# Kernel optimization log

Measured on AMD Instinct MI355X. Metric: run time of the kernel, lower is better.

The kernel has to match this reference:

```python
import jax, jax.numpy as jnp
import numpy as np

N_NODES = 100000
N_EDGES = 1600000
IN_DIM, HID_DIM, OUT_DIM = 128, 256, 128


def gcn_conv(x, src, dst, W, b, n):
    # PyG GCNConv: linear transform, add self-loops, symmetric normalization,
    # scatter-sum aggregation over destination nodes, then bias.
    h = x @ W  # [n, d_out]
    loops = jnp.arange(n, dtype=src.dtype)
    s = jnp.concatenate([src, loops])
    d = jnp.concatenate([dst, loops])
    deg = jax.ops.segment_sum(jnp.ones_like(d, dtype=h.dtype), d, num_segments=n)
    dinv = jnp.where(deg > 0, jax.lax.rsqrt(deg), 0.0)
    norm = dinv[s] * dinv[d]  # [E+n]
    msg = h[s] * norm[:, None]  # gather + scale
    out = jax.ops.segment_sum(msg, d, num_segments=n)  # scatter-reduce
    return out + b


def layer_norm(x, gamma, beta, eps=1e-5):
    mu = jnp.mean(x, axis=-1, keepdims=True)
    var = jnp.mean(jnp.square(x - mu), axis=-1, keepdims=True)
    return (x - mu) * jax.lax.rsqrt(var + eps) * gamma + beta


def setup_inputs() -> dict:
    key = jax.random.key(0)
    ks = jax.random.split(key, 8)
    x = jax.random.normal(ks[0], (N_NODES, IN_DIM), dtype=jnp.float32)
    edge_index = jax.random.randint(ks[1], (2, N_EDGES), 0, N_NODES, dtype=jnp.int64)
    W1 = jax.random.normal(ks[2], (IN_DIM, HID_DIM), dtype=jnp.float32) * (1.0 / np.sqrt(IN_DIM))
    b1 = jnp.zeros((HID_DIM,), dtype=jnp.float32)
    W2 = jax.random.normal(ks[3], (HID_DIM, OUT_DIM), dtype=jnp.float32) * (1.0 / np.sqrt(HID_DIM))
    b2 = jnp.zeros((OUT_DIM,), dtype=jnp.float32)
    gamma = jnp.ones((OUT_DIM,), dtype=jnp.float32)
    beta = jnp.zeros((OUT_DIM,), dtype=jnp.float32)
    return {"x": x, "edge_index": edge_index, "W1": W1, "b1": b1,
            "W2": W2, "b2": b2, "gamma": gamma, "beta": beta}


def reference(x, edge_index, W1, b1, W2, b2, gamma, beta):
    n = x.shape[0]
    src, dst = edge_index[0], edge_index[1]
    h = gcn_conv(x, src, dst, W1, b1, n)
    h = jax.nn.relu(h)
    # dropout(p=0.1) is identity in eval mode
    h = gcn_conv(h, src, dst, W2, b2, n)
    return layer_norm(h, gamma, beta)
```

## Files before the change

### kernel.cpp

```cpp
#include <hip/hip_runtime.h>
#include <hip/hip_fp16.h>
#include <stdint.h>

#define N_NODES 100000
#define N_EDGES 1600000
#define IN_DIM  128
#define HID_DIM 256
#define OUT_DIM 128
#define RS 264
#define NBUCK 782
#define EPB   4096
#define PADB  2816
#define RPT   11
#define PB    391
#define WB    256

typedef __attribute__((ext_vector_type(8))) _Float16 f16x8;
typedef __attribute__((ext_vector_type(4))) float f32x4;

__device__ __forceinline__ int clampi(int v) {
    v = v < 0 ? 0 : v;
    return v >= N_NODES ? N_NODES - 1 : v;
}
__device__ __forceinline__ float2 h2f2(uint32_t u) {
    union { uint32_t u; __half2 h; } c; c.u = u;
    return __half22float2(c.h);
}
__device__ __forceinline__ uint32_t packh(float a, float b) {
    union { __half2 h; uint32_t u; } c; c.h = __floats2half2_rn(a, b);
    return c.u;
}
__device__ __forceinline__ uint16_t f2h(float a) {
    union { __half h; uint16_t s; } c; c.h = __float2half_rn(a);
    return c.s;
}

__device__ __forceinline__ int src_at(const int* ei, int isI64, int e) {
    return clampi(isI64 ? ei[2 * (size_t)e] : ei[e]);
}
__device__ __forceinline__ int dst_at(const int* ei, int isI64, int e) {
    return clampi(isI64 ? ei[2 * (size_t)N_EDGES + 2 * (size_t)e]
                        : ei[(size_t)N_EDGES + e]);
}


__global__ __launch_bounds__(256) void partition_kernel(const int* __restrict__ ei,
                                                        int* __restrict__ cursor,
                                                        uint32_t* __restrict__ recs,
                                                        const float* __restrict__ W1,
                                                        uint16_t* __restrict__ W1t,
                                                        const float* __restrict__ W2,
                                                        uint16_t* __restrict__ W2t) {
    if (blockIdx.x >= PB) {
        int idx = (blockIdx.x - PB) * 256 + threadIdx.x;
        if (idx < IN_DIM * HID_DIM) {
            int k = idx / HID_DIM, n = idx - k * HID_DIM;
            W1t[n * IN_DIM + k] = f2h(W1[idx]);
        } else {
            int j = idx - IN_DIM * HID_DIM;
            int k = j / OUT_DIM, n = j - k * OUT_DIM;
            W2t[n * HID_DIM + k] = f2h(W2[j]);
        }
        return;
    }
    __shared__ int hist[NBUCK];
    __shared__ int gBase[NBUCK];
    __shared__ int s_flag;
    int tid = threadIdx.x;
    if (tid == 0) {
        int z = 1;
        #pragma unroll
        for (int i = 0; i < 16; ++i)
            if (ei[2 * i + 1] != 0) z = 0;
        s_flag = z;
    }
    for (int b = tid; b < NBUCK; b += 256) hist[b] = 0;
    __syncthreads();
    int isI64 = s_flag;
    int base = blockIdx.x * EPB;
    int srcs[16], dsts[16], slots[16];
    #pragma unroll
    for (int r = 0; r < 16; ++r) {
        int e = base + r * 256 + tid;
        slots[r] = -1;
        srcs[r] = 0; dsts[r] = 0;
        if (e < N_EDGES) {
            srcs[r] = src_at(ei, isI64, e);
            dsts[r] = dst_at(ei, isI64, e);
            slots[r] = atomicAdd(&hist[dsts[r] >> 7], 1);
        }
    }
    __syncthreads();
    for (int b = tid; b < NBUCK; b += 256)
        if (hist[b] > 0) gBase[b] = atomicAdd(&cursor[b], hist[b]);
    __syncthreads();
    #pragma unroll
    for (int r = 0; r < 16; ++r) {
        if (slots[r] >= 0) {
            int b = dsts[r] >> 7;
            int pos = gBase[b] + slots[r];
            if (pos < PADB)
                recs[(size_t)b * PADB + pos] =
                    ((uint32_t)srcs[r] << 7) | (uint32_t)(dsts[r] & 127);
        }
    }
}


__global__ __launch_bounds__(256) void build_kernel(const uint32_t* __restrict__ recs,
                                                    const int* __restrict__ cursor,
                                                    int* __restrict__ row_ptr,
                                                    float* __restrict__ dinv,
                                                    int* __restrict__ colv) {
    __shared__ int cnt[128];
    __shared__ int lofs[128];
    __shared__ int cur[128];
    __shared__ int wsum[8];
    int b = blockIdx.x, tid = threadIdx.x;
    int lane = tid & 63, wv = tid >> 6;
    int nb = cursor[b]; if (nb > PADB) nb = PADB;
    int pv = 0;
    for (int j = tid; j < b; j += 256) {
        int c = cursor[j];
        pv += (c > PADB) ? PADB : c;
    }
    #pragma unroll
    for (int o = 32; o > 0; o >>= 1) pv += __shfl_xor(pv, o, 64);
    if (tid < 128) { cnt[tid] = 0; cur[tid] = 0; }
    if (lane == 0) wsum[wv] = pv;
    __syncthreads();
    int cbase = wsum[0] + wsum[1] + wsum[2] + wsum[3];
    uint32_t rr[RPT];
    #pragma unroll
    for (int r = 0; r < RPT; ++r) {
        int i = r * 256 + tid;
        rr[r] = 0xFFFFFFFFu;
        if (i < nb) {
            rr[r] = recs[(size_t)b * PADB + i];
            atomicAdd(&cnt[rr[r] & 127], 1);
        }
    }
    __syncthreads();
    int v = (tid < 128) ? cnt[tid] : 0;
    int inc = v;
    #pragma unroll
    for (int o = 1; o < 64; o <<= 1) {
        int t = __shfl_up(inc, o, 64);
        if (lane >= o) inc += t;
    }
    if (lane == 63) wsum[4 + wv] = inc;
    __syncthreads();
    int woff = 0;
    #pragma unroll
    for (int w = 0; w < 4; ++w) if (w < wv) woff += wsum[4 + w];
    int excl = woff + inc - v;
    int node = b * 128 + tid;
    if (tid < 128) {
        lofs[tid] = excl;
        if (node < N_NODES) {
            row_ptr[node] = cbase + excl;
            dinv[node] = rsqrtf((float)(v + 1));
        }
    }
    if (b == NBUCK - 1 && tid == 0) row_ptr[N_NODES] = cbase + nb;
    __syncthreads();
    #pragma unroll
    for (int r = 0; r < RPT; ++r) {
        if (rr[r] != 0xFFFFFFFFu) {
            int id = (int)(rr[r] & 127);
            int slot = atomicAdd(&cur[id], 1);
            colv[cbase + lofs[id] + slot] = (int)(rr[r] >> 7);
        }
    }
}


__global__ __launch_bounds__(256) void xscale_kernel(const float* __restrict__ x,
                                                     const float* __restrict__ dinv,
                                                     uint2* __restrict__ xs16) {
    int idx = blockIdx.x * 256 + threadIdx.x;
    if (idx < N_NODES * 32) {
        float d = dinv[idx >> 5];
        float4 v = ((const float4*)x)[idx];
        uint2 o;
        o.x = packh(d * v.x, d * v.y);
        o.y = packh(d * v.z, d * v.w);
        xs16[idx] = o;
    }
}


template<bool LN>
__global__ __launch_bounds__(256) void agg_kernel(const uint4* __restrict__ rows,
                                                  const int* __restrict__ row_ptr,
                                                  const int* __restrict__ colv,
                                                  const float* __restrict__ dinv,
                                                  const float* __restrict__ bias,
                                                  const float* __restrict__ gamma,
                                                  const float* __restrict__ beta,
                                                  float* __restrict__ out,
                                                  uint4* __restrict__ out16) {
    int node = blockIdx.x * 16 + (threadIdx.x >> 4);
    if (node >= N_NODES) return;
    int l = threadIdx.x & 15;
    const char* base = (const char*)rows + ((unsigned)l << 4);
    float di = dinv[node];
    float acc[8];
    {
        uint4 u = *(const uint4*)(base + ((unsigned)node << 8));
        float2 f0 = h2f2(u.x), f1 = h2f2(u.y), f2 = h2f2(u.z), f3 = h2f2(u.w);
        acc[0] = f0.x; acc[1] = f0.y; acc[2] = f1.x; acc[3] = f1.y;
        acc[4] = f2.x; acc[5] = f2.y; acc[6] = f3.x; acc[7] = f3.y;
    }
    int e = row_ptr[node], e1 = row_ptr[node + 1];
    int s0 = 0, s1 = 0, s2 = 0, s3 = 0;
    if (e     < e1) s0 = colv[e];
    if (e + 1 < e1) s1 = colv[e + 1];
    if (e + 2 < e1) s2 = colv[e + 2];
    if (e + 3 < e1) s3 = colv[e + 3];
    while (e + 4 <= e1) {
        uint4 v0 = *(const uint4*)(base + ((unsigned)s0 << 8));
        uint4 v1 = *(const uint4*)(base + ((unsigned)s1 << 8));
        uint4 v2 = *(const uint4*)(base + ((unsigned)s2 << 8));
        uint4 v3 = *(const uint4*)(base + ((unsigned)s3 << 8));
        int p0 = (e + 4 < e1) ? e + 4 : e;
        int p1 = (e + 5 < e1) ? e + 5 : e;
        int p2 = (e + 6 < e1) ? e + 6 : e;
        int p3 = (e + 7 < e1) ? e + 7 : e;
        int t0 = colv[p0], t1 = colv[p1], t2 = colv[p2], t3 = colv[p3];
        {
            float2 f0 = h2f2(v0.x), f1 = h2f2(v0.y), f2 = h2f2(v0.z), f3 = h2f2(v0.w);
            acc[0] += f0.x; acc[1] += f0.y; acc[2] += f1.x; acc[3] += f1.y;
            acc[4] += f2.x; acc[5] += f2.y; acc[6] += f3.x; acc[7] += f3.y;
        }
        {
            float2 f0 = h2f2(v1.x), f1 = h2f2(v1.y), f2 = h2f2(v1.z), f3 = h2f2(v1.w);
            acc[0] += f0.x; acc[1] += f0.y; acc[2] += f1.x; acc[3] += f1.y;
            acc[4] += f2.x; acc[5] += f2.y; acc[6] += f3.x; acc[7] += f3.y;
        }
        {
            float2 f0 = h2f2(v2.x), f1 = h2f2(v2.y), f2 = h2f2(v2.z), f3 = h2f2(v2.w);
            acc[0] += f0.x; acc[1] += f0.y; acc[2] += f1.x; acc[3] += f1.y;
            acc[4] += f2.x; acc[5] += f2.y; acc[6] += f3.x; acc[7] += f3.y;
        }
        {
            float2 f0 = h2f2(v3.x), f1 = h2f2(v3.y), f2 = h2f2(v3.z), f3 = h2f2(v3.w);
            acc[0] += f0.x; acc[1] += f0.y; acc[2] += f1.x; acc[3] += f1.y;
            acc[4] += f2.x; acc[5] += f2.y; acc[6] += f3.x; acc[7] += f3.y;
        }
        s0 = t0; s1 = t1; s2 = t2; s3 = t3; e += 4;
    }
    int r = e1 - e;
    if (r > 0) {
        uint4 v = *(const uint4*)(base + ((unsigned)s0 << 8));
        float2 f0 = h2f2(v.x), f1 = h2f2(v.y), f2 = h2f2(v.z), f3 = h2f2(v.w);
        acc[0] += f0.x; acc[1] += f0.y; acc[2] += f1.x; acc[3] += f1.y;
        acc[4] += f2.x; acc[5] += f2.y; acc[6] += f3.x; acc[7] += f3.y;
    }
    if (r > 1) {
        uint4 v = *(const uint4*)(base + ((unsigned)s1 << 8));
        float2 f0 = h2f2(v.x), f1 = h2f2(v.y), f2 = h2f2(v.z), f3 = h2f2(v.w);
        acc[0] += f0.x; acc[1] += f0.y; acc[2] += f1.x; acc[3] += f1.y;
        acc[4] += f2.x; acc[5] += f2.y; acc[6] += f3.x; acc[7] += f3.y;
    }
    if (r > 2) {
        uint4 v = *(const uint4*)(base + ((unsigned)s2 << 8));
        float2 f0 = h2f2(v.x), f1 = h2f2(v.y), f2 = h2f2(v.z), f3 = h2f2(v.w);
        acc[0] += f0.x; acc[1] += f0.y; acc[2] += f1.x; acc[3] += f1.y;
        acc[4] += f2.x; acc[5] += f2.y; acc[6] += f3.x; acc[7] += f3.y;
    }
    if (!LN) {
        uint4 o;
        o.x = packh(acc[0] * di, acc[1] * di);
        o.y = packh(acc[2] * di, acc[3] * di);
        o.z = packh(acc[4] * di, acc[5] * di);
        o.w = packh(acc[6] * di, acc[7] * di);
        out16[(size_t)node * 16 + l] = o;
    } else {
        const float4* b4 = (const float4*)(bias + l * 8);
        float4 bb0 = b4[0], bb1 = b4[1];
        float v[8];
        v[0] = acc[0] * di + bb0.x; v[1] = acc[1] * di + bb0.y;
        v[2] = acc[2] * di + bb0.z; v[3] = acc[3] * di + bb0.w;
        v[4] = acc[4] * di + bb1.x; v[5] = acc[5] * di + bb1.y;
        v[6] = acc[6] * di + bb1.z; v[7] = acc[7] * di + bb1.w;
        float s = 0.f;
        #pragma unroll
        for (int j = 0; j < 8; ++j) s += v[j];
        #pragma unroll
        for (int o = 8; o > 0; o >>= 1) s += __shfl_xor(s, o, 64);
        float mu = s * (1.0f / 128.0f);
        float q = 0.f;
        #pragma unroll
        for (int j = 0; j < 8; ++j) { v[j] -= mu; q += v[j] * v[j]; }
        #pragma unroll
        for (int o = 8; o > 0; o >>= 1) q += __shfl_xor(q, o, 64);
        float rstd = rsqrtf(q * (1.0f / 128.0f) + 1e-5f);
        const float4* g4 = (const float4*)(gamma + l * 8);
        const float4* t4 = (const float4*)(beta + l * 8);
        float4 g0 = g4[0], g1 = g4[1], t0 = t4[0], t1 = t4[1];
        float* orow = out + (size_t)node * 128 + l * 8;
        f32x4 o0, o1;
        o0.x = v[0] * rstd * g0.x + t0.x; o0.y = v[1] * rstd * g0.y + t0.y;
        o0.z = v[2] * rstd * g0.z + t0.z; o0.w = v[3] * rstd * g0.w + t0.w;
        o1.x = v[4] * rstd * g1.x + t1.x; o1.y = v[5] * rstd * g1.y + t1.y;
        o1.z = v[6] * rstd * g1.z + t1.z; o1.w = v[7] * rstd * g1.w + t1.w;
        __builtin_nontemporal_store(o0, (f32x4*)orow);
        __builtin_nontemporal_store(o1, (f32x4*)(orow + 4));
    }
}


__global__ __launch_bounds__(256) void fused_gemm_kernel(const uint16_t* __restrict__ A16,
                                                         const uint16_t* __restrict__ W1t,
                                                         const float* __restrict__ b1,
                                                         const uint16_t* __restrict__ W2t,
                                                         const float* __restrict__ dinv,
                                                         uint16_t* __restrict__ G16, int M) {
    __shared__ __align__(16) uint16_t Hs[64 * RS];
    int lane = threadIdx.x & 63;
    int wave = threadIdx.x >> 6;
    int r15 = lane & 15;
    int quad = lane >> 4;
    int kofs = quad * 8;
    int blk_row = blockIdx.x * 64;

    f16x8 a[4][4];
    #pragma unroll
    for (int mt = 0; mt < 4; ++mt) {
        bool valid = (blk_row + mt * 16) < M;
        int row = valid ? (blk_row + mt * 16 + r15) : 0;
        const uint16_t* arow = A16 + (size_t)row * IN_DIM + kofs;
        #pragma unroll
        for (int ks = 0; ks < 4; ++ks)
            a[mt][ks] = *(const f16x8*)(arow + ks * 32);
    }

    #pragma unroll
    for (int nt = 0; nt < 4; ++nt) {
        int ncol = (wave * 4 + nt) * 16 + r15;
        const uint16_t* bp = W1t + (size_t)ncol * IN_DIM + kofs;
        f32x4 acc[4];
        #pragma unroll
        for (int mt = 0; mt < 4; ++mt) acc[mt] = (f32x4){0.f, 0.f, 0.f, 0.f};
        #pragma unroll
        for (int ks = 0; ks < 4; ++ks) {
            f16x8 bv = *(const f16x8*)(bp + ks * 32);
            #pragma unroll
            for (int mt = 0; mt < 4; ++mt)
                acc[mt] = __builtin_amdgcn_mfma_f32_16x16x32_f16(a[mt][ks], bv, acc[mt], 0, 0, 0);
        }
        float bb = b1[ncol];
        #pragma unroll
        for (int mt = 0; mt < 4; ++mt) {
            #pragma unroll
            for (int r = 0; r < 4; ++r) {
                int lrow = mt * 16 + quad * 4 + r;
                Hs[lrow * RS + ncol] = f2h(fmaxf(acc[mt][r] + bb, 0.f));
            }
        }
    }
    __syncthreads();

    #pragma unroll
    for (int nt = 0; nt < 2; ++nt) {
        int ncol = (wave * 2 + nt) * 16 + r15;
        const uint16_t* bp = W2t + (size_t)ncol * HID_DIM + kofs;
        f16x8 b2[8];
        #pragma unroll
        for (int ks = 0; ks < 8; ++ks)
            b2[ks] = *(const f16x8*)(bp + ks * 32);
        f32x4 acc[4];
        #pragma unroll
        for (int mt = 0; mt < 4; ++mt) acc[mt] = (f32x4){0.f, 0.f, 0.f, 0.f};
        #pragma unroll
        for (int ks = 0; ks < 8; ++ks) {
            #pragma unroll
            for (int mt = 0; mt < 4; ++mt) {
                f16x8 av = *(const f16x8*)(Hs + (mt * 16 + r15) * RS + ks * 32 + kofs);
                acc[mt] = __builtin_amdgcn_mfma_f32_16x16x32_f16(av, b2[ks], acc[mt], 0, 0, 0);
            }
        }
        #pragma unroll
        for (int mt = 0; mt < 4; ++mt) {
            if ((blk_row + mt * 16) < M) {
                #pragma unroll
                for (int r = 0; r < 4; ++r) {
                    int row = blk_row + mt * 16 + quad * 4 + r;
                    G16[(size_t)row * OUT_DIM + ncol] = f2h(dinv[row] * acc[mt][r]);
                }
            }
        }
    }
}


extern "C" void kernel_launch(void* const* d_in, const int* in_sizes, int n_in,
                              void* d_out, int out_size, void* d_ws, size_t ws_size,
                              hipStream_t stream) {
    const float* x     = (const float*)d_in[0];
    const int*   ei    = (const int*)d_in[1];
    const float* W1    = (const float*)d_in[2];
    const float* b1    = (const float*)d_in[3];
    const float* W2    = (const float*)d_in[4];
    const float* b2    = (const float*)d_in[5];
    const float* gamma = (const float*)d_in[6];
    const float* beta  = (const float*)d_in[7];

    char* ws = (char*)d_ws;
    size_t off = 0;
    auto alloc = [&](size_t bytes) -> void* {
        void* p = ws + off;
        off += (bytes + 511) & ~(size_t)511;
        return p;
    };
    int*      cursor  = (int*)alloc((size_t)NBUCK * 4);
    int*      row_ptr = (int*)alloc((size_t)(N_NODES + 1) * 4);
    float*    dinv    = (float*)alloc((size_t)N_NODES * 4);
    uint16_t* W1t     = (uint16_t*)alloc((size_t)IN_DIM * HID_DIM * 2);
    uint16_t* W2t     = (uint16_t*)alloc((size_t)HID_DIM * OUT_DIM * 2);
    int*      colv    = (int*)alloc((size_t)N_EDGES * 4);
    void*     big     = alloc((size_t)N_NODES * IN_DIM * 2);
    uint32_t* recs    = (uint32_t*)big;
    uint16_t* g16     = (uint16_t*)big;
    if (ws_size < off) return;

    uint2*    xs16 = (uint2*)d_out;
    uint16_t* xa16 = (uint16_t*)d_out + (size_t)N_NODES * IN_DIM;

    const int AB = (N_NODES + 15) / 16;
    const int GB = (N_NODES + 63) / 64;
    const int XB = (N_NODES * 32 + 255) / 256;

    hipMemsetAsync(cursor, 0, (size_t)NBUCK * 4, stream);
    partition_kernel<<<PB + WB, 256, 0, stream>>>(ei, cursor, recs, W1, W1t, W2, W2t);
    build_kernel<<<NBUCK, 256, 0, stream>>>(recs, cursor, row_ptr, dinv, colv);
    xscale_kernel<<<XB, 256, 0, stream>>>(x, dinv, xs16);
    agg_kernel<false><<<AB, 256, 0, stream>>>((const uint4*)xs16, row_ptr, colv, dinv,
                                              nullptr, nullptr, nullptr,
                                              nullptr, (uint4*)xa16);
    fused_gemm_kernel<<<GB, 256, 0, stream>>>(xa16, W1t, b1, W2t, dinv, g16, N_NODES);
    agg_kernel<true><<<AB, 256, 0, stream>>>((const uint4*)g16, row_ptr, colv, dinv,
                                             b2, gamma, beta, (float*)d_out, nullptr);
}
```

Measured before the change: 315.1 us.

## Slice layer-1 features into column slabs for cache-resident gather aggregation

Stores the scaled fp16 input features as 8 column slices of 16 features each (node-major within a slice) and adds a new first-layer aggregation kernel in which each block handles one slice for 64 nodes, with 4 lanes per node. Because blocks are interleaved by slice, each slice's working set is about 3.2 MB, which is meant to let the random neighbor gathers hit in L2/LLC instead of DRAM. The GEMM's A-operand load is updated to read this sliced layout. In exchange, the CSR column indices are re-read 8 times and each gather is only 8 bytes per lane, which reduces memory-access efficiency per request.

```diff
diff --git a/kernel.cpp b/kernel.cpp
--- a/kernel.cpp
+++ b/kernel.cpp
@@ -14,6 +14,7 @@
 #define RPT   11
 #define PB    391
 #define WB    256
+#define NSL   8
 
 typedef __attribute__((ext_vector_type(8))) _Float16 f16x8;
 typedef __attribute__((ext_vector_type(4))) float f32x4;
@@ -177,16 +178,95 @@
 
 __global__ __launch_bounds__(256) void xscale_kernel(const float* __restrict__ x,
                                                      const float* __restrict__ dinv,
-                                                     uint2* __restrict__ xs16) {
-    int idx = blockIdx.x * 256 + threadIdx.x;
-    if (idx < N_NODES * 32) {
-        float d = dinv[idx >> 5];
-        float4 v = ((const float4*)x)[idx];
+                                                     uint2* __restrict__ xsl) {
+    int T = blockIdx.x * 256 + threadIdx.x;
+    if (T < N_NODES * 32) {
+        int slice = T / (N_NODES * 4);
+        int rem = T - slice * (N_NODES * 4);
+        int node = rem >> 2;
+        int off4 = rem & 3;
+        float d = dinv[node];
+        float4 v = *(const float4*)(x + (size_t)node * 128 + slice * 16 + off4 * 4);
         uint2 o;
         o.x = packh(d * v.x, d * v.y);
         o.y = packh(d * v.z, d * v.w);
-        xs16[idx] = o;
-    }
+        xsl[T] = o;
+    }
+}
+
+
+__global__ __launch_bounds__(256) void agg1s_kernel(const uint2* __restrict__ xsl,
+                                                    const int* __restrict__ row_ptr,
+                                                    const int* __restrict__ colv,
+                                                    const float* __restrict__ dinv,
+                                                    uint2* __restrict__ xal) {
+    int b = blockIdx.x;
+    int s = b & 7;
+    int node = (b >> 3) * 64 + (threadIdx.x >> 2);
+    if (node >= N_NODES) return;
+    int l = threadIdx.x & 3;
+    const uint2* sb = xsl + (size_t)s * (N_NODES * 4) + l;
+    float di = dinv[node];
+    float acc[4];
+    {
+        uint2 u = sb[(unsigned)node * 4];
+        float2 f0 = h2f2(u.x), f1 = h2f2(u.y);
+        acc[0] = f0.x; acc[1] = f0.y; acc[2] = f1.x; acc[3] = f1.y;
+    }
+    int e = row_ptr[node], e1 = row_ptr[node + 1];
+    int s0 = 0, s1 = 0, s2 = 0, s3 = 0;
+    if (e     < e1) s0 = colv[e];
+    if (e + 1 < e1) s1 = colv[e + 1];
+    if (e + 2 < e1) s2 = colv[e + 2];
+    if (e + 3 < e1) s3 = colv[e + 3];
+    while (e + 4 <= e1) {
+        uint2 v0 = sb[(unsigned)s0 * 4];
+        uint2 v1 = sb[(unsigned)s1 * 4];
+        uint2 v2 = sb[(unsigned)s2 * 4];
+        uint2 v3 = sb[(unsigned)s3 * 4];
+        int p0 = (e + 4 < e1) ? e + 4 : e;
+        int p1 = (e + 5 < e1) ? e + 5 : e;
+        int p2 = (e + 6 < e1) ? e + 6 : e;
+        int p3 = (e + 7 < e1) ? e + 7 : e;
+        int t0 = colv[p0], t1 = colv[p1], t2 = colv[p2], t3 = colv[p3];
+        {
+            float2 f0 = h2f2(v0.x), f1 = h2f2(v0.y);
+            acc[0] += f0.x; acc[1] += f0.y; acc[2] += f1.x; acc[3] += f1.y;
+        }
+        {
+            float2 f0 = h2f2(v1.x), f1 = h2f2(v1.y);
+            acc[0] += f0.x; acc[1] += f0.y; acc[2] += f1.x; acc[3] += f1.y;
+        }
+        {
+            float2 f0 = h2f2(v2.x), f1 = h2f2(v2.y);
+            acc[0] += f0.x; acc[1] += f0.y; acc[2] += f1.x; acc[3] += f1.y;
+        }
+        {
+            float2 f0 = h2f2(v3.x), f1 = h2f2(v3.y);
+            acc[0] += f0.x; acc[1] += f0.y; acc[2] += f1.x; acc[3] += f1.y;
+        }
+        s0 = t0; s1 = t1; s2 = t2; s3 = t3; e += 4;
+    }
+    int r = e1 - e;
+    if (r > 0) {
+        uint2 v = sb[(unsigned)s0 * 4];
+        float2 f0 = h2f2(v.x), f1 = h2f2(v.y);
+        acc[0] += f0.x; acc[1] += f0.y; acc[2] += f1.x; acc[3] += f1.y;
+    }
+    if (r > 1) {
+        uint2 v = sb[(unsigned)s1 * 4];
+        float2 f0 = h2f2(v.x), f1 = h2f2(v.y);
+        acc[0] += f0.x; acc[1] += f0.y; acc[2] += f1.x; acc[3] += f1.y;
+    }
+    if (r > 2) {
+        uint2 v = sb[(unsigned)s2 * 4];
+        float2 f0 = h2f2(v.x), f1 = h2f2(v.y);
+        acc[0] += f0.x; acc[1] += f0.y; acc[2] += f1.x; acc[3] += f1.y;
+    }
+    uint2 o;
+    o.x = packh(acc[0] * di, acc[1] * di);
+    o.y = packh(acc[2] * di, acc[3] * di);
+    xal[(size_t)s * (N_NODES * 4) + (unsigned)node * 4 + l] = o;
 }
 
 
@@ -330,10 +410,12 @@
     for (int mt = 0; mt < 4; ++mt) {
         bool valid = (blk_row + mt * 16) < M;
         int row = valid ? (blk_row + mt * 16 + r15) : 0;
-        const uint16_t* arow = A16 + (size_t)row * IN_DIM + kofs;
-        #pragma unroll
-        for (int ks = 0; ks < 4; ++ks)
-            a[mt][ks] = *(const f16x8*)(arow + ks * 32);
+        #pragma unroll
+        for (int ks = 0; ks < 4; ++ks) {
+            int f0 = ks * 32 + kofs;
+            a[mt][ks] = *(const f16x8*)(A16 +
+                ((size_t)(f0 >> 4) * N_NODES + row) * 16 + (f0 & 15));
+        }
     }
 
     #pragma unroll
@@ -425,21 +507,21 @@
     uint16_t* g16     = (uint16_t*)big;
     if (ws_size < off) return;
 
-    uint2*    xs16 = (uint2*)d_out;
-    uint16_t* xa16 = (uint16_t*)d_out + (size_t)N_NODES * IN_DIM;
+    uint2*    xsl = (uint2*)d_out;
+    uint2*    xal = (uint2*)((uint16_t*)d_out + (size_t)N_NODES * IN_DIM);
 
     const int AB = (N_NODES + 15) / 16;
     const int GB = (N_NODES + 63) / 64;
     const int XB = (N_NODES * 32 + 255) / 256;
+    const int SB = ((N_NODES + 63) / 64) * NSL;
 
     hipMemsetAsync(cursor, 0, (size_t)NBUCK * 4, stream);
     partition_kernel<<<PB + WB, 256, 0, stream>>>(ei, cursor, recs, W1, W1t, W2, W2t);
     build_kernel<<<NBUCK, 256, 0, stream>>>(recs, cursor, row_ptr, dinv, colv);
-    xscale_kernel<<<XB, 256, 0, stream>>>(x, dinv, xs16);
-    agg_kernel<false><<<AB, 256, 0, stream>>>((const uint4*)xs16, row_ptr, colv, dinv,
-                                              nullptr, nullptr, nullptr,
-                                              nullptr, (uint4*)xa16);
-    fused_gemm_kernel<<<GB, 256, 0, stream>>>(xa16, W1t, b1, W2t, dinv, g16, N_NODES);
+    xscale_kernel<<<XB, 256, 0, stream>>>(x, dinv, xsl);
+    agg1s_kernel<<<SB, 256, 0, stream>>>(xsl, row_ptr, colv, dinv, xal);
+    fused_gemm_kernel<<<GB, 256, 0, stream>>>((const uint16_t*)xal, W1t, b1, W2t, dinv,
+                                              g16, N_NODES);
     agg_kernel<true><<<AB, 256, 0, stream>>>((const uint4*)g16, row_ptr, colv, dinv,
                                              b2, gamma, beta, (float*)d_out, nullptr);
 }
```

Result: slower. 330.7 us (+5.0%).
